# Performance work log

Measured on AMD Instinct MI355X. Metric: run time of the kernel, lower is better.

Reference implementation:

```python
import jax, jax.numpy as jnp
import numpy as np

B, C, H, W = 64, 32, 112, 112
RANK = 3


def setup_inputs() -> dict:
    key = jax.random.key(0)
    k1, k2, k3, k4, k5 = jax.random.split(key, 5)
    N = H * W  # 12544
    return {
        "x": jax.random.uniform(k1, (B, C, H, W), dtype=jnp.float32),
        "p_buffer": jax.random.normal(k2, (B, N, RANK), dtype=jnp.float32),
        "q_buffer": jax.random.normal(k3, (B, C, RANK), dtype=jnp.float32),
        "grad_p_buffer": jax.random.normal(k4, (B, N, RANK), dtype=jnp.float32),
        "grad_q_buffer": jax.random.normal(k5, (B, C, RANK), dtype=jnp.float32),
        "n_iter": 2,
    }


def _power_svd(X, P, Q, n_iter):
    # X: [b, c, n]; P: [b, n, r]; Q: [b, c, r]
    for i in range(n_iter):
        if i == n_iter - 1:
            P = jnp.linalg.qr(P)[0]  # batched reduced QR, tall-skinny (n x r)
        Q = jnp.einsum('bcn,bnr->bcr', X, P)
        if i == n_iter - 1:
            Q = jnp.linalg.qr(Q)[0]  # batched reduced QR (c x r)
        P = jnp.einsum('bcn,bcr->bnr', X, Q)  # X^T @ Q
    return P, Q


def reference(x, p_buffer, q_buffer, grad_p_buffer, grad_q_buffer, n_iter):
    shape = x.shape
    X = x.reshape(shape[0], shape[1], -1)  # [B, C, H*W]
    P, Q = _power_svd(X, p_buffer, q_buffer, n_iter)
    # low-rank reconstruction Q @ P^T, back to original shape
    return jnp.einsum('bcr,bnr->bcn', Q, P).reshape(shape)
```

## Files before the change

kernel.cpp:

```cpp
#include <hip/hip_runtime.h>
#include <math.h>

#define N_HW 12544
#define TN 128
#define NCH 98

#define WS_QG 65536
#define WS_U  (WS_QG + 64*96)
#define ZTOT  (WS_U)

typedef __attribute__((ext_vector_type(8)))  short short8;
typedef __attribute__((ext_vector_type(16))) float f32x16;
typedef __attribute__((ext_vector_type(4)))  float f32x4;

#define MFMA(a, b, c) __builtin_amdgcn_mfma_f32_32x32x16_bf16((a), (b), (c), 0, 0, 0)

__device__ __forceinline__ void split3(float f, ushort& h, ushort& m, ushort& l) {
    unsigned u = __builtin_bit_cast(unsigned, f);
    h = (ushort)(u >> 16);
    float fh = __builtin_bit_cast(float, u & 0xffff0000u);
    float rm = f - fh;
    unsigned um = __builtin_bit_cast(unsigned, rm);
    m = (ushort)(um >> 16);
    float fm = __builtin_bit_cast(float, um & 0xffff0000u);
    float rl = rm - fm;
    l = (ushort)(__builtin_bit_cast(unsigned, rl) >> 16);
}

__device__ __forceinline__ int xq(int c, int o) {
    return c * 16 + ((o & 8) | ((o ^ c) & 7));
}

__global__ __launch_bounds__(256)
void k0_zero(float* __restrict__ ws)
{
    const int g = blockIdx.x * 256 + threadIdx.x;
    if (g < ZTOT / 4) ((float4*)ws)[g] = make_float4(0.f, 0.f, 0.f, 0.f);
}

__global__ __launch_bounds__(256)
void k1_gram(const float* __restrict__ x, const float* __restrict__ p,
             float* __restrict__ Sg, float* __restrict__ Qg)
{
    const int b = blockIdx.y, j = blockIdx.x;
    const int tid = threadIdx.x;
    const int lane = tid & 63, wave = tid >> 6;
    const int nbase = j * TN;

    __shared__ uint4 XS[3 * 512];
    __shared__ alignas(16) ushort PTH[3 * TN], PTM[3 * TN], PTL[3 * TN];
    __shared__ float Ssum[1024], T2[1024], T3[1024];
    float* dmp = (float*)XS;

    {
        const int c = tid >> 3, oc = tid & 7;
        const float4* xr = (const float4*)(x + ((size_t)b * 32 + c) * N_HW + nbase);
        #pragma unroll
        for (int t = 0; t < 2; ++t) {
            const int o = oc + 8 * t;
            float4 f0 = xr[2 * o], f1 = xr[2 * o + 1];
            float fv[8] = {f0.x, f0.y, f0.z, f0.w, f1.x, f1.y, f1.z, f1.w};
            unsigned hw[4], mw[4], lw[4];
            #pragma unroll
            for (int i = 0; i < 4; ++i) {
                ushort h0, m0, l0, h1, m1, l1;
                split3(fv[2 * i],     h0, m0, l0);
                split3(fv[2 * i + 1], h1, m1, l1);
                hw[i] = (unsigned)h0 | ((unsigned)h1 << 16);
                mw[i] = (unsigned)m0 | ((unsigned)m1 << 16);
                lw[i] = (unsigned)l0 | ((unsigned)l1 << 16);
            }
            const int s = xq(c, o);
            XS[s]        = make_uint4(hw[0], hw[1], hw[2], hw[3]);
            XS[512 + s]  = make_uint4(mw[0], mw[1], mw[2], mw[3]);
            XS[1024 + s] = make_uint4(lw[0], lw[1], lw[2], lw[3]);
        }
    }
    if (tid < TN) {
        const float* pb = p + (size_t)b * N_HW * 3 + (size_t)(nbase + tid) * 3;
        #pragma unroll
        for (int r = 0; r < 3; ++r) {
            ushort h, m, l;
            split3(pb[r], h, m, l);
            PTH[r * TN + tid] = h; PTM[r * TN + tid] = m; PTL[r * TN + tid] = l;
        }
    }
    __syncthreads();

    f32x16 D1 = {0,0,0,0,0,0,0,0,0,0,0,0,0,0,0,0};
    f32x16 D2 = {0,0,0,0,0,0,0,0,0,0,0,0,0,0,0,0};
    f32x16 D3 = {0,0,0,0,0,0,0,0,0,0,0,0,0,0,0,0};
    f32x16 DQ = {0,0,0,0,0,0,0,0,0,0,0,0,0,0,0,0};
    const int cl = lane & 31, g = lane >> 5;
    const int rr = (cl < 3) ? cl : 0;
    for (int s = wave; s < 8; s += 4) {
        const int sl = xq(cl, 2 * s + g);
        short8 xh = __builtin_bit_cast(short8, XS[sl]);
        short8 xm = __builtin_bit_cast(short8, XS[512 + sl]);
        short8 xl = __builtin_bit_cast(short8, XS[1024 + sl]);
        const int po = rr * TN + 16 * s + 8 * g;
        short8 ph = *(const short8*)&PTH[po];
        short8 pm = *(const short8*)&PTM[po];
        short8 pl = *(const short8*)&PTL[po];
        D1 = MFMA(xh, xh, D1);
        D1 = MFMA(xm, xm, D1);
        D2 = MFMA(xh, xm, D2);
        D3 = MFMA(xh, xl, D3);
        DQ = MFMA(xh, ph, DQ);
        DQ = MFMA(xh, pm, DQ);
        DQ = MFMA(xm, ph, DQ);
        DQ = MFMA(xh, pl, DQ);
        DQ = MFMA(xl, ph, DQ);
        DQ = MFMA(xm, pm, DQ);
    }

    #define DUMP_REDUCE(D, dst)                                                            \
        __syncthreads();                                                                   \
        _Pragma("unroll")                                                                  \
        for (int i = 0; i < 4; ++i)                                                        \
            *(float4*)&dmp[tid * 20 + 4 * i] =                                             \
                make_float4((D)[4*i], (D)[4*i+1], (D)[4*i+2], (D)[4*i+3]);                 \
        __syncthreads();                                                                   \
        _Pragma("unroll")                                                                  \
        for (int it = 0; it < 4; ++it) {                                                   \
            const int e = tid + 256 * it;                                                  \
            const int r = e >> 5, co = e & 31;                                             \
            const int ln = co + 32 * ((r >> 2) & 1);                                       \
            const int rg = (r & 3) + 4 * (r >> 3);                                         \
            (dst)[e] = dmp[ln * 20 + rg] + dmp[(64 + ln) * 20 + rg]                        \
                     + dmp[(128 + ln) * 20 + rg] + dmp[(192 + ln) * 20 + rg];              \
        }

    DUMP_REDUCE(D1, Ssum)
    DUMP_REDUCE(D2, T2)
    DUMP_REDUCE(D3, T3)
    __syncthreads();
    {
        float* Sb = Sg + (size_t)b * 1024;
        #pragma unroll
        for (int it = 0; it < 4; ++it) {
            const int e = tid + 256 * it;
            const int r = e >> 5, co = e & 31;
            const int et = (co << 5) | r;
            atomicAdd(&Sb[e], Ssum[e] + T2[e] + T2[et] + T3[e] + T3[et]);
        }
    }
    __syncthreads();
    #pragma unroll
    for (int i = 0; i < 4; ++i)
        *(float4*)&dmp[tid * 20 + 4 * i] = make_float4(DQ[4*i], DQ[4*i+1], DQ[4*i+2], DQ[4*i+3]);
    __syncthreads();
    if (tid < 96) {
        const int c2 = tid / 3, r2 = tid - 3 * c2;
        const int ln = r2 + 32 * ((c2 >> 2) & 1);
        const int rg = (c2 & 3) + 4 * (c2 >> 3);
        float s = dmp[ln * 20 + rg] + dmp[(64 + ln) * 20 + rg]
                + dmp[(128 + ln) * 20 + rg] + dmp[(192 + ln) * 20 + rg];
        atomicAdd(&Qg[(size_t)b * 96 + tid], s);
    }
}

__global__ __launch_bounds__(128)
void k2_solve(const float* __restrict__ Sg, const float* __restrict__ Qg,
              float* __restrict__ Uo)
{
    const int b = blockIdx.x, tid = threadIdx.x;
    __shared__ float S[1024];
    __shared__ float Qv[96];
    __shared__ float V[96];
    __shared__ float G[6], L[6];

    #pragma unroll
    for (int i = 0; i < 8; ++i) S[tid + 128 * i] = Sg[(size_t)b * 1024 + tid + 128 * i];
    if (tid < 96) Qv[tid] = Qg[(size_t)b * 96 + tid];
    __syncthreads();
    if (tid < 96) {
        const int c = tid / 3, r = tid % 3;
        float s = 0.f;
        #pragma unroll 8
        for (int cc = 0; cc < 32; ++cc) s += S[c * 32 + cc] * Qv[cc * 3 + r];
        V[tid] = s;
    }
    for (int round = 0; round < 2; ++round) {
        __syncthreads();
        if (tid < 6) {
            const int r = (tid > 2) ? 2 : ((tid > 0) ? 1 : 0);
            const int s = tid - (r * (r + 1)) / 2;
            float g = 0.f;
            for (int c = 0; c < 32; ++c) g += V[c * 3 + r] * V[c * 3 + s];
            G[tid] = g;
        }
        __syncthreads();
        if (tid == 0) {
            const float l00 = sqrtf(G[0]);
            const float l10 = G[1] / l00, l20 = G[3] / l00;
            const float l11 = sqrtf(G[2] - l10 * l10);
            const float l21 = (G[4] - l20 * l10) / l11;
            const float l22 = sqrtf(G[5] - l20 * l20 - l21 * l21);
            L[0] = l00; L[1] = l10; L[2] = l11; L[3] = l20; L[4] = l21; L[5] = l22;
        }
        __syncthreads();
        if (tid < 32) {
            const float v0 = V[tid * 3 + 0], v1 = V[tid * 3 + 1], v2 = V[tid * 3 + 2];
            const float u0 = v0 / L[0];
            const float u1 = (v1 - L[1] * u0) / L[2];
            const float u2 = (v2 - L[3] * u0 - L[4] * u1) / L[5];
            V[tid * 3 + 0] = u0; V[tid * 3 + 1] = u1; V[tid * 3 + 2] = u2;
        }
    }
    __syncthreads();
    if (tid < 32) {
        Uo[(size_t)b * 128 + tid * 4 + 0] = V[tid * 3 + 0];
        Uo[(size_t)b * 128 + tid * 4 + 1] = V[tid * 3 + 1];
        Uo[(size_t)b * 128 + tid * 4 + 2] = V[tid * 3 + 2];
        Uo[(size_t)b * 128 + tid * 4 + 3] = 0.f;
    }
}

__global__ __launch_bounds__(256)
void k3_out(const float* __restrict__ x, const float* __restrict__ Uw,
            float* __restrict__ out)
{
    const int b = blockIdx.y, tid = threadIdx.x;
    __shared__ float Us[32][4];
    if (tid < 128) ((float*)Us)[tid] = Uw[(size_t)b * 128 + tid];
    __syncthreads();
    const int g = blockIdx.x * 256 + tid;
    if (g >= N_HW / 4) return;

    const float* Xb = x   + (size_t)b * 32 * N_HW + 4 * (size_t)g;
    float*       Ob = out + (size_t)b * 32 * N_HW + 4 * (size_t)g;

    float t0x = 0, t0y = 0, t0z = 0, t0w = 0;
    float t1x = 0, t1y = 0, t1z = 0, t1w = 0;
    float t2x = 0, t2y = 0, t2z = 0, t2w = 0;
    #pragma unroll 16
    for (int c = 0; c < 32; ++c) {
        float4 xv = *(const float4*)(Xb + (size_t)c * N_HW);
        const float u0 = Us[c][0], u1 = Us[c][1], u2 = Us[c][2];
        t0x += u0 * xv.x; t0y += u0 * xv.y; t0z += u0 * xv.z; t0w += u0 * xv.w;
        t1x += u1 * xv.x; t1y += u1 * xv.y; t1z += u1 * xv.z; t1w += u1 * xv.w;
        t2x += u2 * xv.x; t2y += u2 * xv.y; t2z += u2 * xv.z; t2w += u2 * xv.w;
    }
    #pragma unroll 16
    for (int c = 0; c < 32; ++c) {
        const float u0 = Us[c][0], u1 = Us[c][1], u2 = Us[c][2];
        f32x4 o;
        o.x = u0 * t0x + u1 * t1x + u2 * t2x;
        o.y = u0 * t0y + u1 * t1y + u2 * t2y;
        o.z = u0 * t0z + u1 * t1z + u2 * t2z;
        o.w = u0 * t0w + u1 * t1w + u2 * t2w;
        __builtin_nontemporal_store(o, (f32x4*)(Ob + (size_t)c * N_HW));
    }
}

extern "C" void kernel_launch(void* const* d_in, const int* in_sizes, int n_in,
                              void* d_out, int out_size, void* d_ws, size_t ws_size,
                              hipStream_t stream)
{
    const float* x = (const float*)d_in[0];
    const float* p = (const float*)d_in[1];
    float* ws = (float*)d_ws;
    float* Sg = ws;
    float* Qg = ws + WS_QG;
    float* U  = ws + WS_U;
    float* out = (float*)d_out;

    hipLaunchKernelGGL(k0_zero, dim3((ZTOT / 4 + 255) / 256), dim3(256), 0, stream, ws);
    hipLaunchKernelGGL(k1_gram, dim3(NCH, 64), dim3(256), 0, stream, x, p, Sg, Qg);
    hipLaunchKernelGGL(k2_solve, dim3(64), dim3(128), 0, stream, Sg, Qg, U);
    hipLaunchKernelGGL(k3_out, dim3((N_HW / 4 + 255) / 256, 64), dim3(256), 0, stream, x, U, out);
}
```

Before: 250.4 us.

## Make gram kernel persistent over column chunks with register prefetch

The gram kernel's grid shrinks from 98 chunk-blocks per batch to 16 blocks per batch, each looping over chunks with stride 16. Each block keeps its MFMA accumulators across chunks, and it loads the next chunk's x and p values into registers while the current chunk is being computed. This cuts the number of per-block reductions and atomic/partial writes and overlaps global loads with compute. The cost is fewer blocks in flight (1024 in total), an uneven chunk count per block (98/16), and an extra barrier per iteration.

```diff
diff --git a/kernel.cpp b/kernel.cpp
--- a/kernel.cpp
+++ b/kernel.cpp
@@ -4,6 +4,7 @@
 #define N_HW 12544
 #define TN 128
 #define NCH 98
+#define KB 16
 
 #define WS_QG 65536
 #define WS_U  (WS_QG + 64*96)
@@ -42,23 +43,44 @@
 void k1_gram(const float* __restrict__ x, const float* __restrict__ p,
              float* __restrict__ Sg, float* __restrict__ Qg)
 {
-    const int b = blockIdx.y, j = blockIdx.x;
+    const int b = blockIdx.y, kb = blockIdx.x;
     const int tid = threadIdx.x;
     const int lane = tid & 63, wave = tid >> 6;
-    const int nbase = j * TN;
 
     __shared__ uint4 XS[3 * 512];
     __shared__ alignas(16) ushort PTH[3 * TN], PTM[3 * TN], PTL[3 * TN];
     __shared__ float Ssum[1024], T2[1024], T3[1024];
     float* dmp = (float*)XS;
 
+    const int c = tid >> 3, oc = tid & 7;
+    const float* xrow = x + ((size_t)b * 32 + c) * N_HW;
+    const float* pbat = p + (size_t)b * N_HW * 3;
+
+    f32x16 D1 = {0,0,0,0,0,0,0,0,0,0,0,0,0,0,0,0};
+    f32x16 D2 = {0,0,0,0,0,0,0,0,0,0,0,0,0,0,0,0};
+    f32x16 D3 = {0,0,0,0,0,0,0,0,0,0,0,0,0,0,0,0};
+    f32x16 DQ = {0,0,0,0,0,0,0,0,0,0,0,0,0,0,0,0};
+    const int cl = lane & 31, g = lane >> 5;
+    const int rr = (cl < 3) ? cl : 0;
+
+    float4 pre[4];
+    float prep[3];
+    int j = kb;
     {
-        const int c = tid >> 3, oc = tid & 7;
-        const float4* xr = (const float4*)(x + ((size_t)b * 32 + c) * N_HW + nbase);
+        const float4* xr = (const float4*)(xrow + (size_t)j * TN);
+        pre[0] = xr[2 * oc];      pre[1] = xr[2 * oc + 1];
+        pre[2] = xr[2 * oc + 16]; pre[3] = xr[2 * oc + 17];
+        if (tid < TN) {
+            const float* pb = pbat + (size_t)(j * TN + tid) * 3;
+            prep[0] = pb[0]; prep[1] = pb[1]; prep[2] = pb[2];
+        }
+    }
+
+    while (true) {
         #pragma unroll
         for (int t = 0; t < 2; ++t) {
             const int o = oc + 8 * t;
-            float4 f0 = xr[2 * o], f1 = xr[2 * o + 1];
+            float4 f0 = pre[2 * t], f1 = pre[2 * t + 1];
             float fv[8] = {f0.x, f0.y, f0.z, f0.w, f1.x, f1.y, f1.z, f1.w};
             unsigned hw[4], mw[4], lw[4];
             #pragma unroll
@@ -75,43 +97,52 @@
             XS[512 + s]  = make_uint4(mw[0], mw[1], mw[2], mw[3]);
             XS[1024 + s] = make_uint4(lw[0], lw[1], lw[2], lw[3]);
         }
-    }
-    if (tid < TN) {
-        const float* pb = p + (size_t)b * N_HW * 3 + (size_t)(nbase + tid) * 3;
-        #pragma unroll
-        for (int r = 0; r < 3; ++r) {
-            ushort h, m, l;
-            split3(pb[r], h, m, l);
-            PTH[r * TN + tid] = h; PTM[r * TN + tid] = m; PTL[r * TN + tid] = l;
-        }
-    }
-    __syncthreads();
-
-    f32x16 D1 = {0,0,0,0,0,0,0,0,0,0,0,0,0,0,0,0};
-    f32x16 D2 = {0,0,0,0,0,0,0,0,0,0,0,0,0,0,0,0};
-    f32x16 D3 = {0,0,0,0,0,0,0,0,0,0,0,0,0,0,0,0};
-    f32x16 DQ = {0,0,0,0,0,0,0,0,0,0,0,0,0,0,0,0};
-    const int cl = lane & 31, g = lane >> 5;
-    const int rr = (cl < 3) ? cl : 0;
-    for (int s = wave; s < 8; s += 4) {
-        const int sl = xq(cl, 2 * s + g);
-        short8 xh = __builtin_bit_cast(short8, XS[sl]);
-        short8 xm = __builtin_bit_cast(short8, XS[512 + sl]);
-        short8 xl = __builtin_bit_cast(short8, XS[1024 + sl]);
-        const int po = rr * TN + 16 * s + 8 * g;
-        short8 ph = *(const short8*)&PTH[po];
-        short8 pm = *(const short8*)&PTM[po];
-        short8 pl = *(const short8*)&PTL[po];
-        D1 = MFMA(xh, xh, D1);
-        D1 = MFMA(xm, xm, D1);
-        D2 = MFMA(xh, xm, D2);
-        D3 = MFMA(xh, xl, D3);
-        DQ = MFMA(xh, ph, DQ);
-        DQ = MFMA(xh, pm, DQ);
-        DQ = MFMA(xm, ph, DQ);
-        DQ = MFMA(xh, pl, DQ);
-        DQ = MFMA(xl, ph, DQ);
-        DQ = MFMA(xm, pm, DQ);
+        if (tid < TN) {
+            #pragma unroll
+            for (int r = 0; r < 3; ++r) {
+                ushort h, m, l;
+                split3(prep[r], h, m, l);
+                PTH[r * TN + tid] = h; PTM[r * TN + tid] = m; PTL[r * TN + tid] = l;
+            }
+        }
+
+        const int jn = j + KB;
+        const bool more = (jn < NCH);
+        if (more) {
+            const float4* xr = (const float4*)(xrow + (size_t)jn * TN);
+            pre[0] = xr[2 * oc];      pre[1] = xr[2 * oc + 1];
+            pre[2] = xr[2 * oc + 16]; pre[3] = xr[2 * oc + 17];
+            if (tid < TN) {
+                const float* pb = pbat + (size_t)(jn * TN + tid) * 3;
+                prep[0] = pb[0]; prep[1] = pb[1]; prep[2] = pb[2];
+            }
+        }
+        __syncthreads();
+
+        for (int s = wave; s < 8; s += 4) {
+            const int sl = xq(cl, 2 * s + g);
+            short8 xh = __builtin_bit_cast(short8, XS[sl]);
+            short8 xm = __builtin_bit_cast(short8, XS[512 + sl]);
+            short8 xl = __builtin_bit_cast(short8, XS[1024 + sl]);
+            const int po = rr * TN + 16 * s + 8 * g;
+            short8 ph = *(const short8*)&PTH[po];
+            short8 pm = *(const short8*)&PTM[po];
+            short8 pl = *(const short8*)&PTL[po];
+            D1 = MFMA(xh, xh, D1);
+            D1 = MFMA(xm, xm, D1);
+            D2 = MFMA(xh, xm, D2);
+            D3 = MFMA(xh, xl, D3);
+            DQ = MFMA(xh, ph, DQ);
+            DQ = MFMA(xh, pm, DQ);
+            DQ = MFMA(xm, ph, DQ);
+            DQ = MFMA(xh, pl, DQ);
+            DQ = MFMA(xl, ph, DQ);
+            DQ = MFMA(xm, pm, DQ);
+        }
+
+        if (!more) break;
+        j = jn;
+        __syncthreads();
     }
 
     #define DUMP_REDUCE(D, dst)                                                            \
@@ -267,7 +298,7 @@
     float* out = (float*)d_out;
 
     hipLaunchKernelGGL(k0_zero, dim3((ZTOT / 4 + 255) / 256), dim3(256), 0, stream, ws);
-    hipLaunchKernelGGL(k1_gram, dim3(NCH, 64), dim3(256), 0, stream, x, p, Sg, Qg);
+    hipLaunchKernelGGL(k1_gram, dim3(KB, 64), dim3(256), 0, stream, x, p, Sg, Qg);
     hipLaunchKernelGGL(k2_solve, dim3(64), dim3(128), 0, stream, Sg, Qg, U);
     hipLaunchKernelGGL(k3_out, dim3((N_HW / 4 + 255) / 256, 64), dim3(256), 0, stream, x, U, out);
 }
```

New measurement: 232.5 us. -7.1%, faster.
